# Kernel tuning notes

Measured on AMD Instinct MI355X. Metric: run time of the kernel, lower is better.

The kernel has to match this reference:

```python
import jax, jax.numpy as jnp
import numpy as np

N_NODES = 50000
N_EDGES = 800000
HIDDEN = 128
BN_EPS = 1e-5
LEAKY_SLOPE = 0.01


def setup_inputs() -> dict:
    key = jax.random.key(0)
    ks = jax.random.split(key, 8)
    x = jax.random.normal(ks[0], (N_NODES, HIDDEN), dtype=jnp.float32)
    edge_index = jax.random.randint(ks[1], (2, N_EDGES), 0, N_NODES, dtype=jnp.int64)
    # stacked per-layer params (4 SAGEConv layers, all 128->128)
    sc = 1.0 / np.sqrt(HIDDEN)
    Wl = jax.random.normal(ks[2], (4, HIDDEN, HIDDEN), dtype=jnp.float32) * sc
    bl = jax.random.normal(ks[3], (4, HIDDEN), dtype=jnp.float32) * sc
    Wr = jax.random.normal(ks[4], (4, HIDDEN, HIDDEN), dtype=jnp.float32) * sc
    gamma = jnp.ones((4, HIDDEN), dtype=jnp.float32)
    beta = jnp.zeros((4, HIDDEN), dtype=jnp.float32)
    return {"x": x, "edge_index": edge_index, "Wl": Wl, "bl": bl,
            "Wr": Wr, "gamma": gamma, "beta": beta}


def _sage_mean_agg(x, src, dst, n):
    # gather source features per edge, scatter-mean onto destination nodes
    msg = x[src]                                                  # [E, F]
    agg = jax.ops.segment_sum(msg, dst, num_segments=n)           # [N, F]
    cnt = jax.ops.segment_sum(jnp.ones_like(dst, dtype=x.dtype), dst, num_segments=n)
    return agg / jnp.maximum(cnt, 1.0)[:, None]


def _bn_train(x, g, b):
    mu = jnp.mean(x, axis=0)
    var = jnp.mean((x - mu) ** 2, axis=0)  # biased variance (PyTorch BN normalization)
    return (x - mu) * jax.lax.rsqrt(var + BN_EPS) * g + b


def reference(x, edge_index, Wl, bl, Wr, gamma, beta):
    src, dst = edge_index[0], edge_index[1]
    n = x.shape[0]
    h = x
    for i in range(4):
        agg = _sage_mean_agg(h, src, dst, n)
        h = agg @ Wl[i] + bl[i] + h @ Wr[i]          # SAGEConv: lin_l(mean_nbr) + lin_r(root)
        h = jnp.where(h >= 0, h, LEAKY_SLOPE * h)    # leaky_relu
        h = _bn_train(h, gamma[i], beta[i])
    # dropout: eval-mode identity (deterministic reference)
    return h
```

## Files before the change

kernel.cpp:

```cpp
#include <hip/hip_runtime.h>
#include <hip/hip_bf16.h>

#define N_NODES 50000
#define N_EDGES 800000
#define F 128
#define BN_EPS 1e-5f
#define SLOPE 0.01f
#define NB 782
#define GBLK 104
#define CAP 64

typedef __attribute__((ext_vector_type(8))) __bf16 bf16x8_t;
typedef __attribute__((ext_vector_type(8))) unsigned short u16x8_t;
typedef __attribute__((ext_vector_type(4))) float f32x4_t;

__device__ __forceinline__ unsigned short f2b(float f) {
    unsigned int u = __float_as_uint(f);
    unsigned int r = (u + 0x7fffu + ((u >> 16) & 1u)) >> 16;
    return (unsigned short)r;
}
__device__ __forceinline__ float b2f_lo(unsigned int v) { return __uint_as_float(v << 16); }
__device__ __forceinline__ float b2f_hi(unsigned int v) { return __uint_as_float(v & 0xffff0000u); }


__global__ void build_kernel(const int* __restrict__ src, const int* __restrict__ dst,
                             int* __restrict__ deg, unsigned short* __restrict__ csr) {
    const int g = blockIdx.x & 7;
    const int bg = blockIdx.x >> 3;
    const int lo = g * (N_NODES / 8), hi = lo + (N_NODES / 8);
    for (int e = bg * 256 + threadIdx.x; e < N_EDGES; e += GBLK * 256) {
        int d = __builtin_nontemporal_load(dst + e);
        if (d >= lo && d < hi) {
            int s = __builtin_nontemporal_load(src + e);
            int pos = atomicAdd(&deg[d], 1);
            if (pos < CAP) csr[d * CAP + pos] = (unsigned short)s;
        }
    }
}


__global__ __launch_bounds__(256) void f2b_kernel(const float* __restrict__ in,
                                                  unsigned short* __restrict__ out) {
    long i = (long)blockIdx.x * blockDim.x + threadIdx.x;
    if (i >= (long)N_NODES * (F / 4)) return;
    float4 v = ((const float4*)in)[i];
    ushort4 o;
    o.x = f2b(v.x); o.y = f2b(v.y); o.z = f2b(v.z); o.w = f2b(v.w);
    ((ushort4*)out)[i] = o;
}

__global__ __launch_bounds__(256) void wprep_kernel(const float* __restrict__ Wl,
                                                    const float* __restrict__ Wr,
                                                    unsigned short* __restrict__ Wt) {
    int idx = blockIdx.x * blockDim.x + threadIdx.x;
    if (idx >= 4 * F * 256) return;
    int k = idx & 255;
    int n = (idx >> 8) & 127;
    int i = idx >> 15;
    float v = (k < F) ? Wl[((long)i * F + k) * F + n] : Wr[((long)i * F + (k - F)) * F + n];
    Wt[idx] = f2b(v);
}

__global__ void ident_kernel(float* __restrict__ scale, float* __restrict__ shift) {
    int j = threadIdx.x;
    if (j < F) { scale[j] = 1.f; shift[j] = 0.f; }
}


__global__ __launch_bounds__(256) void agg_kernel(const unsigned short* __restrict__ h,
                                                  const int* __restrict__ deg,
                                                  const unsigned short* __restrict__ csr,
                                                  const float* __restrict__ scale,
                                                  const float* __restrict__ shift,
                                                  unsigned short* __restrict__ agg) {
    int node = (int)((blockIdx.x * (unsigned)blockDim.x + threadIdx.x) >> 6);
    int lane = threadIdx.x & 63;
    if (node >= N_NODES) return;
    const int d = deg[node];
    const int beg = node * CAP;
    const int end = beg + d;
    const unsigned short* hl = h + lane * 2;
    float ax = 0.f, ay = 0.f;
    for (int e = beg; e < end; e += 16) {
        int idx[16];
#pragma unroll
        for (int j = 0; j < 16; ++j) {
            int ee = e + j;
            idx[j] = (int)csr[(ee < end) ? ee : beg];
        }
        unsigned int v[16];
#pragma unroll
        for (int j = 0; j < 16; ++j)
            v[j] = *(const unsigned int*)(hl + (long)idx[j] * F);
#pragma unroll
        for (int j = 0; j < 16; ++j) {
            unsigned int m = (e + j < end) ? v[j] : 0u;
            ax += b2f_lo(m);
            ay += b2f_hi(m);
        }
    }
    if (d > 0) {
        const float inv = 1.0f / (float)d;
        const float2 sc = ((const float2*)scale)[lane];
        const float2 sh = ((const float2*)shift)[lane];
        ax = ax * inv * sc.x + sh.x;
        ay = ay * inv * sc.y + sh.y;
    } else {
        ax = 0.f; ay = 0.f;
    }
    unsigned int o = (unsigned int)f2b(ax) | ((unsigned int)f2b(ay) << 16);
    *(unsigned int*)(agg + (long)node * F + lane * 2) = o;
}

__device__ __forceinline__ u16x8_t affine8(u16x8_t av, const float* __restrict__ sc,
                                           const float* __restrict__ sh) {
    u16x8_t r;
#pragma unroll
    for (int j = 0; j < 8; ++j) {
        float v = __uint_as_float(((unsigned int)av[j]) << 16);
        v = v * sc[j] + sh[j];
        r[j] = f2b(v);
    }
    return r;
}

__global__ __launch_bounds__(256) void gemm_mfma(const unsigned short* __restrict__ aggb,
                                                 const unsigned short* __restrict__ hin,
                                                 const float* __restrict__ scale,
                                                 const float* __restrict__ shift,
                                                 const unsigned short* __restrict__ Wt,
                                                 const float* __restrict__ bl,
                                                 float* __restrict__ Pf,
                                                 unsigned short* __restrict__ Pb,
                                                 int write_bf16,
                                                 float* __restrict__ partial) {
    __shared__ __align__(16) char shraw[64 * 136 * 4];
    unsigned short* stage = (unsigned short*)shraw;
    unsigned short* ep16 = (unsigned short*)shraw;
    float* ep32 = (float*)shraw;
    __shared__ float lsum[4][F];
    __shared__ float lsq[4][F];

    const int tid = threadIdx.x;
    const int wave = tid >> 6, lane = tid & 63;
    const int m = lane & 15, q = lane >> 4;
    const int rbase = blockIdx.x * 64 + wave * 16;
    const int arow = rbase + m;
    const bool aval = arow < N_NODES;
    const unsigned short* ap = aggb + (long)arow * F + q * 8;
    const unsigned short* hp = hin + (long)arow * F + q * 8;

    u16x8_t areg[8];
#pragma unroll
    for (int j = 0; j < 8; ++j) areg[j] = (u16x8_t)0;
    if (aval) {
#pragma unroll
        for (int j = 0; j < 4; ++j) areg[j] = *(const u16x8_t*)(ap + j * 32);
#pragma unroll
        for (int j = 0; j < 4; ++j) {
            u16x8_t raw = *(const u16x8_t*)(hp + j * 32);
            const int base = j * 32 + q * 8;
            areg[4 + j] = affine8(raw, scale + base, shift + base);
        }
    }

    f32x4_t acc[8];
#pragma unroll
    for (int nt = 0; nt < 8; ++nt) acc[nt] = (f32x4_t){0.f, 0.f, 0.f, 0.f};

    for (int half = 0; half < 2; ++half) {
        if (half) __syncthreads();
#pragma unroll
        for (int f = 0; f < 8; ++f) {
            const int fid = f * 256 + tid;
            const int lf = fid & 63;
            const int ksf = (fid >> 6) & 3;
            const int ntf = fid >> 8;
            const int n = ntf * 16 + (lf & 15);
            const int k = half * 128 + ksf * 32 + (lf >> 4) * 8;
            *(u16x8_t*)(stage + fid * 8) = *(const u16x8_t*)(Wt + (long)n * 256 + k);
        }
        __syncthreads();
#pragma unroll
        for (int ks = 0; ks < 4; ++ks) {
            bf16x8_t af = __builtin_bit_cast(bf16x8_t, areg[half * 4 + ks]);
#pragma unroll
            for (int nt = 0; nt < 8; ++nt) {
                u16x8_t bv = *(const u16x8_t*)(stage + ((nt * 4 + ks) * 64 + lane) * 8);
                bf16x8_t bf = __builtin_bit_cast(bf16x8_t, bv);
                acc[nt] = __builtin_amdgcn_mfma_f32_16x16x32_bf16(af, bf, acc[nt], 0, 0, 0);
            }
        }
    }

    __syncthreads();

    float cs[8], cq[8];
#pragma unroll
    for (int nt = 0; nt < 8; ++nt) {
        cs[nt] = 0.f; cq[nt] = 0.f;
        const int c = nt * 16 + m;
        const float b = bl[c];
#pragma unroll
        for (int r = 0; r < 4; ++r) {
            const int rl = wave * 16 + q * 4 + r;
            float v = acc[nt][r] + b;
            v = (v >= 0.f) ? v : SLOPE * v;
            if (write_bf16) ep16[rl * 136 + c] = f2b(v);
            else            ep32[rl * 136 + c] = v;
            if (rbase + q * 4 + r < N_NODES) {
                cs[nt] += v;
                cq[nt] += v * v;
            }
        }
    }

    {
        const int rq = lane >> 4;
        const int cc = (lane & 15) * 8;
#pragma unroll
        for (int r2 = 0; r2 < 4; ++r2) {
            const int rl = wave * 16 + rq * 4 + r2;
            const int grow = blockIdx.x * 64 + rl;
            if (grow < N_NODES) {
                if (write_bf16) {
                    *(u16x8_t*)(Pb + (long)grow * F + cc) =
                        *(const u16x8_t*)(ep16 + rl * 136 + cc);
                } else {
                    *(f32x4_t*)(Pf + (long)grow * F + cc) =
                        *(const f32x4_t*)(ep32 + rl * 136 + cc);
                    *(f32x4_t*)(Pf + (long)grow * F + cc + 4) =
                        *(const f32x4_t*)(ep32 + rl * 136 + cc + 4);
                }
            }
        }
    }

#pragma unroll
    for (int nt = 0; nt < 8; ++nt) {
        cs[nt] += __shfl_xor(cs[nt], 16);
        cs[nt] += __shfl_xor(cs[nt], 32);
        cq[nt] += __shfl_xor(cq[nt], 16);
        cq[nt] += __shfl_xor(cq[nt], 32);
    }
    if (lane < 16) {
#pragma unroll
        for (int nt = 0; nt < 8; ++nt) {
            lsum[wave][nt * 16 + m] = cs[nt];
            lsq[wave][nt * 16 + m] = cq[nt];
        }
    }
    __syncthreads();
    if (tid < F) {
        float s = 0.f, s2 = 0.f;
#pragma unroll
        for (int w = 0; w < 4; ++w) {
            s += lsum[w][tid];
            s2 += lsq[w][tid];
        }
        partial[(long)blockIdx.x * 256 + tid] = s;
        partial[(long)blockIdx.x * 256 + 128 + tid] = s2;
    }
}

__global__ __launch_bounds__(256) void bn_reduce(const float* __restrict__ partial,
                                                 const float* __restrict__ gamma,
                                                 const float* __restrict__ beta,
                                                 float* __restrict__ scale,
                                                 float* __restrict__ shift) {
    const int j = blockIdx.x;
    const int t = threadIdx.x;
    const int lane = t & 63, wave = t >> 6;
    float s = 0.f, s2 = 0.f;
    for (int b = t; b < NB; b += 256) {
        s += partial[(long)b * 256 + j];
        s2 += partial[(long)b * 256 + 128 + j];
    }
#pragma unroll
    for (int off = 1; off < 64; off <<= 1) {
        s += __shfl_xor(s, off);
        s2 += __shfl_xor(s2, off);
    }
    __shared__ float ls[4], lq[4];
    if (lane == 0) { ls[wave] = s; lq[wave] = s2; }
    __syncthreads();
    if (t == 0) {
        float S = ls[0] + ls[1] + ls[2] + ls[3];
        float Q = lq[0] + lq[1] + lq[2] + lq[3];
        const float inv_n = 1.0f / (float)N_NODES;
        float mu = S * inv_n;
        float var = Q * inv_n - mu * mu;
        float scl = gamma[j] * rsqrtf(var + BN_EPS);
        scale[j] = scl;
        shift[j] = beta[j] - mu * scl;
    }
}

__global__ __launch_bounds__(256) void bn_apply_f(float* __restrict__ P,
                                                  const float* __restrict__ scale,
                                                  const float* __restrict__ shift) {
    long i = (long)blockIdx.x * blockDim.x + threadIdx.x;
    if (i >= (long)N_NODES * (F / 4)) return;
    const int c4 = (int)(i & 31);
    float4 v = ((float4*)P)[i];
    const float4 sc = ((const float4*)scale)[c4];
    const float4 sh = ((const float4*)shift)[c4];
    v.x = v.x * sc.x + sh.x;
    v.y = v.y * sc.y + sh.y;
    v.z = v.z * sc.z + sh.z;
    v.w = v.w * sc.w + sh.w;
    ((float4*)P)[i] = v;
}


extern "C" void kernel_launch(void* const* d_in, const int* in_sizes, int n_in,
                              void* d_out, int out_size, void* d_ws, size_t ws_size,
                              hipStream_t stream) {
    const float* x     = (const float*)d_in[0];
    const int*   ei    = (const int*)d_in[1];
    const float* Wl    = (const float*)d_in[2];
    const float* bl    = (const float*)d_in[3];
    const float* Wr    = (const float*)d_in[4];
    const float* gamma = (const float*)d_in[5];
    const float* beta  = (const float*)d_in[6];
    float* out = (float*)d_out;

    const int* src = ei;
    const int* dst = ei + N_EDGES;

    char* w = (char*)d_ws;
    auto alloc = [&](size_t bytes) -> char* {
        char* p = w;
        w += (bytes + 255) & ~(size_t)255;
        return p;
    };
    unsigned short* hbA   = (unsigned short*)alloc((size_t)N_NODES * F * 2);
    unsigned short* hbB   = (unsigned short*)alloc((size_t)N_NODES * F * 2);
    unsigned short* aggb  = (unsigned short*)alloc((size_t)N_NODES * F * 2);
    unsigned short* Wt    = (unsigned short*)alloc((size_t)4 * F * 256 * 2);
    int*   deg      = (int*)alloc((size_t)N_NODES * 4);
    unsigned short* csr = (unsigned short*)alloc((size_t)N_NODES * CAP * 2);
    float* partial  = (float*)alloc((size_t)NB * 256 * 4);
    float* scale    = (float*)alloc(F * 4);
    float* shift    = (float*)alloc(F * 4);

    hipMemsetAsync(deg, 0, (size_t)N_NODES * 4, stream);

    build_kernel<<<8 * GBLK, 256, 0, stream>>>(src, dst, deg, csr);

    const int n4 = N_NODES * (F / 4);
    f2b_kernel<<<(n4 + 255) / 256, 256, 0, stream>>>(x, hbA);
    wprep_kernel<<<(4 * F * 256 + 255) / 256, 256, 0, stream>>>(Wl, Wr, Wt);
    ident_kernel<<<1, 128, 0, stream>>>(scale, shift);

    unsigned short* hin = hbA;
    unsigned short* hnext = hbB;
    for (int i = 0; i < 4; ++i) {
        const int last = (i == 3);

        agg_kernel<<<(N_NODES + 3) / 4, 256, 0, stream>>>(hin, deg, csr, scale, shift, aggb);

        gemm_mfma<<<NB, 256, 0, stream>>>(
            aggb, hin, scale, shift, Wt + (size_t)i * F * 256, bl + (size_t)i * F,
            out, hnext, last ? 0 : 1, partial);

        bn_reduce<<<F, 256, 0, stream>>>(partial, gamma + (size_t)i * F, beta + (size_t)i * F,
                                         scale, shift);

        unsigned short* t = hin; hin = hnext; hnext = t;
    }
    bn_apply_f<<<(n4 + 255) / 256, 256, 0, stream>>>(out, scale, shift);
}
```

Measured before the change: 394.9 us.

## Two-pass CSR build: bucket edges by destination group, then scatter with padded counters

Replaces the single CSR build kernel, where each of 8 node groups rescanned the whole edge list, with two passes. A bucketing pass reads edges once, packs (dst,src) into 32-bit words and uses wave-level LDS bins to append them to per-group queues. A scatter pass then fills the CSR from those queues. Degree counters are padded to 64 bytes each to cut atomic contention and false sharing, at the cost of a larger memset, an extra launch, and strided degree reads in the aggregation kernel.

```diff
diff --git a/kernel.cpp b/kernel.cpp
--- a/kernel.cpp
+++ b/kernel.cpp
@@ -7,8 +7,13 @@
 #define BN_EPS 1e-5f
 #define SLOPE 0.01f
 #define NB 782
-#define GBLK 104
 #define CAP 64
+#define NGRP 8
+#define GSZ (N_NODES / NGRP)
+#define QCAP 131072
+#define ABLK 128
+#define AITER ((N_EDGES + ABLK * 256 - 1) / (ABLK * 256))
+#define SBLK 512
 
 typedef __attribute__((ext_vector_type(8))) __bf16 bf16x8_t;
 typedef __attribute__((ext_vector_type(8))) unsigned short u16x8_t;
@@ -22,19 +27,78 @@
 __device__ __forceinline__ float b2f_lo(unsigned int v) { return __uint_as_float(v << 16); }
 __device__ __forceinline__ float b2f_hi(unsigned int v) { return __uint_as_float(v & 0xffff0000u); }
 
-
-__global__ void build_kernel(const int* __restrict__ src, const int* __restrict__ dst,
-                             int* __restrict__ deg, unsigned short* __restrict__ csr) {
+__global__ __launch_bounds__(256) void bucket_kernel(const int* __restrict__ src,
+                                                     const int* __restrict__ dst,
+                                                     int* __restrict__ qtail,
+                                                     unsigned int* __restrict__ qdata) {
+    __shared__ unsigned int bins[4][NGRP][128];
+    const int tid = threadIdx.x;
+    const int lane = tid & 63;
+    const int w = tid >> 6;
+    int bc[NGRP];
+#pragma unroll
+    for (int k = 0; k < NGRP; ++k) bc[k] = 0;
+
+    const int stride = ABLK * 256;
+    for (int it = 0; it < AITER; ++it) {
+        const int e = blockIdx.x * 256 + tid + it * stride;
+        const bool valid = e < N_EDGES;
+        int g = -1;
+        unsigned int pack = 0;
+        if (valid) {
+            int d = __builtin_nontemporal_load(dst + e);
+            int s = __builtin_nontemporal_load(src + e);
+            g = d / GSZ;
+            pack = ((unsigned int)d << 16) | (unsigned int)s;
+        }
+#pragma unroll
+        for (int k = 0; k < NGRP; ++k) {
+            unsigned long long mask = __ballot(g == k);
+            int cnt = __popcll(mask);
+            if (!cnt) continue;
+            int cur = bc[k];
+            if (cur + cnt > 128) {
+                int qb = 0;
+                if (lane == 0) qb = atomicAdd(&qtail[k * 16], cur);
+                qb = __shfl(qb, 0);
+                for (int j = lane; j < cur; j += 64)
+                    qdata[(long)k * QCAP + qb + j] = bins[w][k][j];
+                cur = 0;
+            }
+            if (g == k) {
+                int rank = __popcll(mask & ((1ull << lane) - 1ull));
+                bins[w][k][cur + rank] = pack;
+            }
+            bc[k] = cur + cnt;
+        }
+    }
+#pragma unroll
+    for (int k = 0; k < NGRP; ++k) {
+        int cur = bc[k];
+        if (cur) {
+            int qb = 0;
+            if (lane == 0) qb = atomicAdd(&qtail[k * 16], cur);
+            qb = __shfl(qb, 0);
+            for (int j = lane; j < cur; j += 64)
+                qdata[(long)k * QCAP + qb + j] = bins[w][k][j];
+        }
+    }
+}
+
+__global__ void scatter_kernel(const unsigned int* __restrict__ qdata,
+                               const int* __restrict__ qtail,
+                               int* __restrict__ deg_pad,
+                               unsigned short* __restrict__ csr) {
     const int g = blockIdx.x & 7;
     const int bg = blockIdx.x >> 3;
-    const int lo = g * (N_NODES / 8), hi = lo + (N_NODES / 8);
-    for (int e = bg * 256 + threadIdx.x; e < N_EDGES; e += GBLK * 256) {
-        int d = __builtin_nontemporal_load(dst + e);
-        if (d >= lo && d < hi) {
-            int s = __builtin_nontemporal_load(src + e);
-            int pos = atomicAdd(&deg[d], 1);
-            if (pos < CAP) csr[d * CAP + pos] = (unsigned short)s;
-        }
+    const int n = qtail[g * 16];
+    const unsigned int* q = qdata + (long)g * QCAP;
+    for (int i = bg * 256 + threadIdx.x; i < n; i += (SBLK / 8) * 256) {
+        unsigned int p = __builtin_nontemporal_load(q + i);
+        int d = p >> 16;
+        int s = p & 0xffff;
+        int pos = atomicAdd(&deg_pad[d * 16], 1);
+        if (pos < CAP) csr[d * CAP + pos] = (unsigned short)s;
     }
 }
 
@@ -68,7 +132,7 @@
 
 
 __global__ __launch_bounds__(256) void agg_kernel(const unsigned short* __restrict__ h,
-                                                  const int* __restrict__ deg,
+                                                  const int* __restrict__ deg_pad,
                                                   const unsigned short* __restrict__ csr,
                                                   const float* __restrict__ scale,
                                                   const float* __restrict__ shift,
@@ -76,7 +140,7 @@
     int node = (int)((blockIdx.x * (unsigned)blockDim.x + threadIdx.x) >> 6);
     int lane = threadIdx.x & 63;
     if (node >= N_NODES) return;
-    const int d = deg[node];
+    const int d = deg_pad[node * 16];
     const int beg = node * CAP;
     const int end = beg + d;
     const unsigned short* hl = h + lane * 2;
@@ -338,15 +402,18 @@
     unsigned short* hbB   = (unsigned short*)alloc((size_t)N_NODES * F * 2);
     unsigned short* aggb  = (unsigned short*)alloc((size_t)N_NODES * F * 2);
     unsigned short* Wt    = (unsigned short*)alloc((size_t)4 * F * 256 * 2);
-    int*   deg      = (int*)alloc((size_t)N_NODES * 4);
+    int*   deg_pad  = (int*)alloc((size_t)N_NODES * 16 * 4);
+    int*   qtail    = (int*)alloc(8 * 16 * 4);
+    unsigned int* qdata = (unsigned int*)alloc((size_t)NGRP * QCAP * 4);
     unsigned short* csr = (unsigned short*)alloc((size_t)N_NODES * CAP * 2);
     float* partial  = (float*)alloc((size_t)NB * 256 * 4);
     float* scale    = (float*)alloc(F * 4);
     float* shift    = (float*)alloc(F * 4);
 
-    hipMemsetAsync(deg, 0, (size_t)N_NODES * 4, stream);
-
-    build_kernel<<<8 * GBLK, 256, 0, stream>>>(src, dst, deg, csr);
+    hipMemsetAsync(deg_pad, 0, (size_t)N_NODES * 16 * 4 + 8 * 16 * 4, stream);
+
+    bucket_kernel<<<ABLK, 256, 0, stream>>>(src, dst, qtail, qdata);
+    scatter_kernel<<<SBLK, 256, 0, stream>>>(qdata, qtail, deg_pad, csr);
 
     const int n4 = N_NODES * (F / 4);
     f2b_kernel<<<(n4 + 255) / 256, 256, 0, stream>>>(x, hbA);
@@ -358,7 +425,7 @@
     for (int i = 0; i < 4; ++i) {
         const int last = (i == 3);
 
-        agg_kernel<<<(N_NODES + 3) / 4, 256, 0, stream>>>(hin, deg, csr, scale, shift, aggb);
+        agg_kernel<<<(N_NODES + 3) / 4, 256, 0, stream>>>(hin, deg_pad, csr, scale, shift, aggb);
 
         gemm_mfma<<<NB, 256, 0, stream>>>(
             aggb, hin, scale, shift, Wt + (size_t)i * F * 256, bl + (size_t)i * F,
```

Result: slower. 416.5 us (+5.5%).

## Build CSR via two-pass binning with shared-memory staging per node bin

Applied to the files above, without the earlier changes.

Replaces the single-pass CSR build, in which eight node-range groups each rescanned all edges and used global atomics per edge, with two passes. The first pass packs each (dst,src) pair, counts per destination bin in shared memory, and appends it to one of 128 global queues using one atomic per bin per block. The second pass gives each bin to its own block, which builds per-node adjacency lists in LDS and writes them out with vector stores. Edge-list rereads and global atomic contention are reduced, at the cost of an extra kernel launch and fixed queue capacities that assume roughly uniform destination distribution (each bin has up to 8192 slots).

```diff
diff --git a/kernel.cpp b/kernel.cpp
--- a/kernel.cpp
+++ b/kernel.cpp
@@ -7,8 +7,12 @@
 #define BN_EPS 1e-5f
 #define SLOPE 0.01f
 #define NB 782
-#define GBLK 104
 #define CAP 64
+#define NBIN 128
+#define BINSZ 391
+#define QCAP2 8192
+#define ABLK 512
+#define AITER 7
 
 typedef __attribute__((ext_vector_type(8))) __bf16 bf16x8_t;
 typedef __attribute__((ext_vector_type(8))) unsigned short u16x8_t;
@@ -22,20 +26,78 @@
 __device__ __forceinline__ float b2f_lo(unsigned int v) { return __uint_as_float(v << 16); }
 __device__ __forceinline__ float b2f_hi(unsigned int v) { return __uint_as_float(v & 0xffff0000u); }
 
-
-__global__ void build_kernel(const int* __restrict__ src, const int* __restrict__ dst,
-                             int* __restrict__ deg, unsigned short* __restrict__ csr) {
-    const int g = blockIdx.x & 7;
-    const int bg = blockIdx.x >> 3;
-    const int lo = g * (N_NODES / 8), hi = lo + (N_NODES / 8);
-    for (int e = bg * 256 + threadIdx.x; e < N_EDGES; e += GBLK * 256) {
-        int d = __builtin_nontemporal_load(dst + e);
-        if (d >= lo && d < hi) {
+__global__ __launch_bounds__(256) void bucket2_kernel(const int* __restrict__ src,
+                                                      const int* __restrict__ dst,
+                                                      int* __restrict__ qtail,
+                                                      unsigned int* __restrict__ qdata) {
+    __shared__ int counts[NBIN];
+    __shared__ int cur[NBIN];
+    __shared__ int base[NBIN];
+    const int tid = threadIdx.x;
+
+    for (int k = tid; k < NBIN; k += 256) { counts[k] = 0; cur[k] = 0; }
+    __syncthreads();
+
+    unsigned int pack[AITER];
+    int bin[AITER];
+    const int stride = ABLK * 256;
+#pragma unroll
+    for (int it = 0; it < AITER; ++it) {
+        const int e = blockIdx.x * 256 + tid + it * stride;
+        bin[it] = -1;
+        if (e < N_EDGES) {
+            int d = __builtin_nontemporal_load(dst + e);
             int s = __builtin_nontemporal_load(src + e);
-            int pos = atomicAdd(&deg[d], 1);
-            if (pos < CAP) csr[d * CAP + pos] = (unsigned short)s;
-        }
-    }
+            bin[it] = d / BINSZ;
+            pack[it] = ((unsigned int)d << 16) | (unsigned int)s;
+            atomicAdd(&counts[bin[it]], 1);
+        }
+    }
+    __syncthreads();
+    if (tid < NBIN) {
+        int c = counts[tid];
+        base[tid] = (c > 0) ? atomicAdd(&qtail[tid * 16], c) : 0;
+    }
+    __syncthreads();
+#pragma unroll
+    for (int it = 0; it < AITER; ++it) {
+        if (bin[it] >= 0) {
+            int slot = base[bin[it]] + atomicAdd(&cur[bin[it]], 1);
+            qdata[(long)bin[it] * QCAP2 + slot] = pack[it];
+        }
+    }
+}
+
+__global__ __launch_bounds__(256) void scatter2_kernel(const unsigned int* __restrict__ qdata,
+                                                       const int* __restrict__ qtail,
+                                                       int* __restrict__ deg,
+                                                       unsigned short* __restrict__ csr) {
+    __shared__ int cnt[BINSZ];
+    __shared__ unsigned short stage[BINSZ][CAP];
+    const int b = blockIdx.x;
+    const int nbase = b * BINSZ;
+    const int nn = min(BINSZ, N_NODES - nbase);
+    const int tid = threadIdx.x;
+
+    for (int r = tid; r < BINSZ; r += 256) cnt[r] = 0;
+    __syncthreads();
+
+    const int n = qtail[b * 16];
+    const unsigned int* q = qdata + (long)b * QCAP2;
+    for (int i = tid; i < n; i += 256) {
+        unsigned int p = q[i];
+        int local = (int)(p >> 16) - nbase;
+        int pos = atomicAdd(&cnt[local], 1);
+        if (pos < CAP) stage[local][pos] = (unsigned short)(p & 0xffff);
+    }
+    __syncthreads();
+
+    for (int c = tid; c < nn * (CAP / 8); c += 256) {
+        const int r = c >> 3;
+        const int col = (c & 7) * 8;
+        *(u16x8_t*)(csr + (long)(nbase + r) * CAP + col) = *(const u16x8_t*)&stage[r][col];
+    }
+    for (int r = tid; r < nn; r += 256) deg[nbase + r] = min(cnt[r], CAP);
 }
 
 
@@ -339,14 +401,17 @@
     unsigned short* aggb  = (unsigned short*)alloc((size_t)N_NODES * F * 2);
     unsigned short* Wt    = (unsigned short*)alloc((size_t)4 * F * 256 * 2);
     int*   deg      = (int*)alloc((size_t)N_NODES * 4);
+    int*   qtail    = (int*)alloc((size_t)NBIN * 16 * 4);
+    unsigned int* qdata = (unsigned int*)alloc((size_t)NBIN * QCAP2 * 4);
     unsigned short* csr = (unsigned short*)alloc((size_t)N_NODES * CAP * 2);
     float* partial  = (float*)alloc((size_t)NB * 256 * 4);
     float* scale    = (float*)alloc(F * 4);
     float* shift    = (float*)alloc(F * 4);
 
-    hipMemsetAsync(deg, 0, (size_t)N_NODES * 4, stream);
-
-    build_kernel<<<8 * GBLK, 256, 0, stream>>>(src, dst, deg, csr);
+    hipMemsetAsync(qtail, 0, (size_t)NBIN * 16 * 4, stream);
+
+    bucket2_kernel<<<ABLK, 256, 0, stream>>>(src, dst, qtail, qdata);
+    scatter2_kernel<<<NBIN, 256, 0, stream>>>(qdata, qtail, deg, csr);
 
     const int n4 = N_NODES * (F / 4);
     f2b_kernel<<<(n4 + 255) / 256, 256, 0, stream>>>(x, hbA);
```

Result: faster. 368.5 us (-6.7%).
